# Kernel tuning notes

Hardware: AMD Instinct MI355X
Metric: run time of the kernel (lower is better)

The kernel has to match this reference:

```python
import jax, jax.numpy as jnp
import numpy as np

TOP_K = 2
BALANCE_W = 0.01


def setup_inputs() -> dict:
    key = jax.random.key(0)
    ks = jax.random.split(key, 9)
    B, T, D, E, H, S = 4, 2048, 1024, 16, 1024, 2

    def w(k, shape):
        return jax.random.normal(k, shape, jnp.float32) * 0.02

    return {
        "x": jax.random.normal(ks[0], (B, T, D), jnp.float32),
        "router_w": w(ks[1], (D, E)),
        "router_bias": jnp.zeros((E,), jnp.float32),
        "Wg": w(ks[2], (E, D, H)),
        "Wu": w(ks[3], (E, D, H)),
        "Wd": w(ks[4], (E, H, D)),
        "sWg": w(ks[5], (D, S * H)),
        "sWu": w(ks[6], (D, S * H)),
        "sWd": w(ks[7], (S * H, D)),
    }


def reference(x, router_w, router_bias, Wg, Wu, Wd, sWg, sWu, sWd):
    B, T, D = x.shape
    E = router_w.shape[1]
    flat = x.reshape(-1, D)                      # [N, D], N = B*T
    N = flat.shape[0]

    # ---- router (fp32, matching x.float() in torch ref) ----
    logits = flat @ router_w                     # [N, E]
    probs = jax.nn.softmax(logits, axis=-1)      # unbiased probs
    _, indices = jax.lax.top_k(logits + router_bias, TOP_K)  # [N, K]
    weights = jnp.take_along_axis(probs, indices, axis=-1)   # [N, K]
    weights = weights / jnp.maximum(weights.sum(-1, keepdims=True), 1e-9)

    # per-(token, expert) combine weight; top-k indices are unique per row
    C = jnp.zeros((N, E), flat.dtype).at[jnp.arange(N)[:, None], indices].add(weights)
    expert_load = jax.nn.one_hot(indices, E, dtype=jnp.float32).sum((0, 1))  # [E]

    # ---- routed SwiGLU experts: scan over experts, masked combine ----
    def body(acc, per_e):
        wg, wu, wd, c = per_e                    # [D,H],[D,H],[H,D],[N]
        h = jax.nn.silu(flat @ wg) * (flat @ wu) # [N, H]
        return acc + (h @ wd) * c[:, None], None

    routed, _ = jax.lax.scan(body, jnp.zeros_like(flat), (Wg, Wu, Wd, C.T))

    # ---- shared expert ----
    shared = (jax.nn.silu(flat @ sWg) * (flat @ sWu)) @ sWd

    out = (routed + shared).reshape(B, T, D)

    # ---- Switch/DeepSeek balance loss (training mode) ----
    expert_fraction = expert_load / (N * TOP_K)
    probability_fraction = probs.mean(0)
    balance = BALANCE_W * E * jnp.sum(expert_fraction * probability_fraction)

    return out, balance, expert_load
```

## Files before the change

### kernel.cpp

```cpp
#include <hip/hip_runtime.h>
#include <stdint.h>

#define N_TOK 8192
#define DDIM  1024
#define NEXP  16
#define HDIM  1024
#define SHDIM 2048
#define TM 128
#define BK 64
#define MT_R 144

#define SH_GU_NT  (SHDIM / 64)
#define SH_GU_WGS ((N_TOK / TM) * SH_GU_NT)
#define RT_GU_NT  (HDIM / 64)
#define RT_GU_WGS (MT_R * RT_GU_NT)
#define GU_WGS    (SH_GU_WGS + RT_GU_WGS)

#define TND 128
#define DN_NT     (DDIM / TND)
#define SH_DN_WGS ((N_TOK / TM) * DN_NT)
#define RT_DN_WGS (MT_R * DN_NT)
#define DN_WGS    (SH_DN_WGS + RT_DN_WGS)

#define CPAD 16

typedef __bf16 bf16x8 __attribute__((ext_vector_type(8)));
typedef float  f32x4  __attribute__((ext_vector_type(4)));

__device__ __forceinline__ unsigned short f2bf(float f) {
  union { float f; unsigned u; } v; v.f = f;
  unsigned r = v.u + 0x7fffu + ((v.u >> 16) & 1u);
  return (unsigned short)(r >> 16);
}

__device__ __forceinline__ void gload16(const void* g, void* l) {
  __builtin_amdgcn_global_load_lds(
      (const __attribute__((address_space(1))) void*)g,
      (__attribute__((address_space(3))) void*)l, 16, 0, 0);
}

__device__ __forceinline__ int xcd_swizzle() {
  int nwg = (int)gridDim.x;
  int b = (int)blockIdx.x;
  return (b & 7) * (nwg >> 3) + (b >> 3);
}


__global__ void k_zero(int* cnt, int* cursor, float* probsum) {
  int t = threadIdx.x;
  if (t < NEXP * CPAD) { cnt[t] = 0; cursor[t] = 0; probsum[t] = 0.f; }
}

__global__ __launch_bounds__(256) void k_router(
    const float* __restrict__ x, const float* __restrict__ rw,
    const float* __restrict__ rb, int* __restrict__ cnt,
    int* __restrict__ tok_idx, float* __restrict__ tok_w,
    float* __restrict__ probs) {
  __shared__ float rwT[NEXP * 1024];
  const int t = threadIdx.x;
  {
    int dbase = t >> 2, e0 = (t & 3) * 4;
#pragma unroll
    for (int c = 0; c < 16; c++) {
      int d = dbase + 64 * c;
      float4 v = *(const float4*)(rw + (size_t)d * NEXP + e0);
      rwT[(e0 + 0) * 1024 + d] = v.x;
      rwT[(e0 + 1) * 1024 + d] = v.y;
      rwT[(e0 + 2) * 1024 + d] = v.z;
      rwT[(e0 + 3) * 1024 + d] = v.w;
    }
  }
  __syncthreads();
  const int lane = t & 63, wv = t >> 6;
  const int tok0 = blockIdx.x * 16 + wv * 4;
  float acc[4][NEXP];
#pragma unroll
  for (int tt = 0; tt < 4; tt++)
#pragma unroll
    for (int e = 0; e < NEXP; e++) acc[tt][e] = 0.f;

#pragma unroll
  for (int c = 0; c < 4; c++) {
    int d = lane * 4 + 256 * c;
    float4 xv[4];
#pragma unroll
    for (int tt = 0; tt < 4; tt++)
      xv[tt] = *(const float4*)(x + (size_t)(tok0 + tt) * DDIM + d);
#pragma unroll
    for (int e = 0; e < NEXP; e++) {
      float4 w4 = *(const float4*)(&rwT[e * 1024 + d]);
#pragma unroll
      for (int tt = 0; tt < 4; tt++) {
        acc[tt][e] = fmaf(xv[tt].x, w4.x, acc[tt][e]);
        acc[tt][e] = fmaf(xv[tt].y, w4.y, acc[tt][e]);
        acc[tt][e] = fmaf(xv[tt].z, w4.z, acc[tt][e]);
        acc[tt][e] = fmaf(xv[tt].w, w4.w, acc[tt][e]);
      }
    }
  }
#pragma unroll
  for (int tt = 0; tt < 4; tt++)
#pragma unroll
    for (int e = 0; e < NEXP; e++) {
      float v = acc[tt][e];
#pragma unroll
      for (int o = 32; o; o >>= 1) v += __shfl_xor(v, o);
      acc[tt][e] = v;
    }

#pragma unroll
  for (int tt = 0; tt < 4; tt++) {
    if (lane == tt) {
      int tok = tok0 + tt;
      float mx = acc[tt][0];
#pragma unroll
      for (int e = 1; e < NEXP; e++) mx = fmaxf(mx, acc[tt][e]);
      float p[NEXP]; float s = 0.f;
#pragma unroll
      for (int e = 0; e < NEXP; e++) { p[e] = __expf(acc[tt][e] - mx); s += p[e]; }
      float inv = 1.f / s;
      float* pdst = probs + (size_t)tok * NEXP;
#pragma unroll
      for (int e = 0; e < NEXP; e++) { p[e] *= inv; pdst[e] = p[e]; }
      int i0 = 0; float b0 = acc[tt][0] + rb[0];
#pragma unroll
      for (int e = 1; e < NEXP; e++) { float v = acc[tt][e] + rb[e]; if (v > b0) { b0 = v; i0 = e; } }
      int i1 = -1; float b1 = -3.4e38f;
#pragma unroll
      for (int e = 0; e < NEXP; e++) {
        if (e == i0) continue;
        float v = acc[tt][e] + rb[e]; if (v > b1) { b1 = v; i1 = e; }
      }
      float w0 = 0.f, w1 = 0.f;
#pragma unroll
      for (int e = 0; e < NEXP; e++) { if (e == i0) w0 = p[e]; if (e == i1) w1 = p[e]; }
      float ssum = fmaxf(w0 + w1, 1e-9f);
      w0 /= ssum; w1 /= ssum;
      atomicAdd(&cnt[i0 * CPAD], 1); atomicAdd(&cnt[i1 * CPAD], 1);
      tok_idx[tok * 2]     = i0; tok_idx[tok * 2 + 1] = i1;
      tok_w[tok * 2]       = w0; tok_w[tok * 2 + 1]   = w1;
    }
  }
}

__global__ __launch_bounds__(256) void k_psum(
    const float* __restrict__ probs, float* __restrict__ probsum) {
  __shared__ float ps[NEXP];
  const int t = threadIdx.x;
  if (t < NEXP) ps[t] = 0.f;
  __syncthreads();
  int e = t & 15, trow = t >> 4;
  float s = 0.f;
#pragma unroll
  for (int c = 0; c < 8; c++) {
    int tok = blockIdx.x * 128 + c * 16 + trow;
    s += probs[(size_t)tok * NEXP + e];
  }
  atomicAdd(&ps[e], s);
  __syncthreads();
  if (t < NEXP) atomicAdd(&probsum[t * CPAD], ps[t]);
}

__global__ void k_prefix(const int* __restrict__ cnt, int* __restrict__ offs) {
  if (threadIdx.x == 0) {
    int o = 0;
    for (int e = 0; e < NEXP; e++) { offs[e] = o; o += ((cnt[e * CPAD] + 127) & ~127); }
    offs[NEXP] = o;
  }
}

__global__ __launch_bounds__(256) void k_assign(
    const int* __restrict__ tok_idx, const float* __restrict__ tok_w,
    int* __restrict__ cursor, const int* __restrict__ offs,
    int* __restrict__ row_token, float* __restrict__ row_w) {
  int i = blockIdx.x * 256 + threadIdx.x;
  if (i >= N_TOK * 2) return;
  int e = tok_idx[i];
  int pos = atomicAdd(&cursor[e * CPAD], 1);
  int row = offs[e] + pos;
  row_token[row] = i >> 1;
  row_w[row] = tok_w[i];
}

__global__ void k_f32_to_bf16(const float* __restrict__ src,
                              unsigned short* __restrict__ dst, int n4) {
  int i = blockIdx.x * blockDim.x + threadIdx.x;
  if (i >= n4) return;
  float4 v = ((const float4*)src)[i];
  ushort4 o;
  o.x = f2bf(v.x); o.y = f2bf(v.y); o.z = f2bf(v.z); o.w = f2bf(v.w);
  ((ushort4*)dst)[i] = o;
}

__global__ __launch_bounds__(256) void k_transpose2(
    const float* __restrict__ src, unsigned short* __restrict__ dst, int R, int C) {
  __shared__ float tile[64 * 65];
  size_t mat = (size_t)blockIdx.z * R * C;
  src += mat; dst += mat;
  int tc = blockIdx.x * 64, tr = blockIdx.y * 64;
  int rx = threadIdx.x >> 4;
  int cx = (threadIdx.x & 15) * 4;
#pragma unroll
  for (int p = 0; p < 4; p++) {
    int r = p * 16 + rx;
    float4 v = *(const float4*)(src + (size_t)(tr + r) * C + tc + cx);
    tile[(cx + 0) * 65 + r] = v.x;
    tile[(cx + 1) * 65 + r] = v.y;
    tile[(cx + 2) * 65 + r] = v.z;
    tile[(cx + 3) * 65 + r] = v.w;
  }
  __syncthreads();
#pragma unroll
  for (int p = 0; p < 4; p++) {
    int c = p * 16 + rx;
    float v0 = tile[c * 65 + cx + 0];
    float v1 = tile[c * 65 + cx + 1];
    float v2 = tile[c * 65 + cx + 2];
    float v3 = tile[c * 65 + cx + 3];
    ushort4 o; o.x = f2bf(v0); o.y = f2bf(v1); o.z = f2bf(v2); o.w = f2bf(v3);
    *(ushort4*)(dst + (size_t)(tc + c) * R + tr + cx) = o;
  }
}


__global__ __launch_bounds__(256, 4) void k_gateup_all(
    const unsigned short* __restrict__ Xbf,
    const unsigned short* __restrict__ sWgT,
    const unsigned short* __restrict__ sWuT,
    const unsigned short* __restrict__ WgT,
    const unsigned short* __restrict__ WuT,
    unsigned short* __restrict__ Hs,
    unsigned short* __restrict__ Hr,
    const int* __restrict__ offs, const int* __restrict__ cnt,
    const int* __restrict__ row_token) {
  __shared__ unsigned short As[TM * BK];
  __shared__ unsigned short Bgs[64 * BK];
  __shared__ unsigned short Bus[64 * BK];

  const int wg = xcd_swizzle();
  const int t = threadIdx.x;
  const int lane = t & 63, wv = t >> 6;
  const int lr  = lane >> 3;
  const int kbx = (lane & 7) ^ lr;

  int tm, tn, validEnd, Nh;
  const unsigned short *Bgp, *Bup;
  unsigned short* Hout;
  const unsigned short* pA[4];

  if (wg < SH_GU_WGS) {
    tm = (wg / SH_GU_NT) * TM;
    tn = (wg % SH_GU_NT) * 64;
    validEnd = 0x7fffffff;
    Bgp = sWgT; Bup = sWuT;
    Hout = Hs; Nh = SHDIM;
#pragma unroll
    for (int j = 0; j < 4; j++)
      pA[j] = Xbf + (size_t)(tm + (wv * 4 + j) * 8 + lr) * DDIM;
  } else {
    int wgr = wg - SH_GU_WGS;
    tm = (wgr / RT_GU_NT) * TM;
    tn = (wgr % RT_GU_NT) * 64;
    if (tm >= offs[NEXP]) return;
    int e = 0;
#pragma unroll
    for (int i = 1; i < NEXP; i++) if (tm >= offs[i]) e = i;
    validEnd = offs[e] + cnt[e * CPAD];
    Bgp = WgT + (size_t)e * HDIM * DDIM;
    Bup = WuT + (size_t)e * HDIM * DDIM;
    Hout = Hr; Nh = HDIM;
#pragma unroll
    for (int j = 0; j < 4; j++) {
      int row = tm + (wv * 4 + j) * 8 + lr;
      int tok = row < validEnd ? row_token[row] : 0;
      pA[j] = Xbf + (size_t)tok * DDIM;
    }
  }
  const unsigned short* pBg[2];
  const unsigned short* pBu[2];
#pragma unroll
  for (int j = 0; j < 2; j++) {
    int row = tn + (wv * 2 + j) * 8 + lr;
    pBg[j] = Bgp + (size_t)row * DDIM;
    pBu[j] = Bup + (size_t)row * DDIM;
  }

  auto stage = [&](int k0) {
#pragma unroll
    for (int j = 0; j < 4; j++)
      gload16(pA[j] + k0 + kbx * 8, (void*)&As[(wv * 4 + j) * 512]);
#pragma unroll
    for (int j = 0; j < 2; j++) {
      gload16(pBg[j] + k0 + kbx * 8, (void*)&Bgs[(wv * 2 + j) * 512]);
      gload16(pBu[j] + k0 + kbx * 8, (void*)&Bus[(wv * 2 + j) * 512]);
    }
  };

  f32x4 accG[4][2] = {};
  f32x4 accU[4][2] = {};
  const int wr = wv >> 1, wc = wv & 1;
  const int rbase = lane & 15;
  const int kgrp = lane >> 4;

  for (int k0 = 0; k0 < DDIM; k0 += BK) {
    if (k0) __syncthreads();
    stage(k0);
    __syncthreads();
#pragma unroll
    for (int kk = 0; kk < 2; kk++) {
      bf16x8 af[4], gf[2], uf[2];
      int kbl = kk * 4 + kgrp;
#pragma unroll
      for (int i = 0; i < 4; i++) {
        int r = wr * 64 + i * 16 + rbase;
        af[i] = *(const bf16x8*)((const char*)&As[0] + r * 128 + ((kbl ^ (r & 7)) << 4));
      }
#pragma unroll
      for (int j = 0; j < 2; j++) {
        int r = wc * 32 + j * 16 + rbase;
        gf[j] = *(const bf16x8*)((const char*)&Bgs[0] + r * 128 + ((kbl ^ (r & 7)) << 4));
        uf[j] = *(const bf16x8*)((const char*)&Bus[0] + r * 128 + ((kbl ^ (r & 7)) << 4));
      }
#pragma unroll
      for (int i = 0; i < 4; i++)
#pragma unroll
        for (int j = 0; j < 2; j++) {
          accG[i][j] = __builtin_amdgcn_mfma_f32_16x16x32_bf16(af[i], gf[j], accG[i][j], 0, 0, 0);
          accU[i][j] = __builtin_amdgcn_mfma_f32_16x16x32_bf16(af[i], uf[j], accU[i][j], 0, 0, 0);
        }
    }
  }

  const int orow0 = tm + wr * 64 + (lane >> 4) * 4;
  const int ocol0 = tn + wc * 32 + (lane & 15);
#pragma unroll
  for (int i = 0; i < 4; i++)
#pragma unroll
    for (int j = 0; j < 2; j++)
#pragma unroll
      for (int r = 0; r < 4; r++) {
        int row = orow0 + i * 16 + r;
        if (row < validEnd) {
          float g = accG[i][j][r], u = accU[i][j][r];
          float h = g / (1.f + __expf(-g)) * u;
          Hout[(size_t)row * Nh + ocol0 + j * 16] = f2bf(h);
        }
      }
}

__global__ __launch_bounds__(256, 4) void k_down_all(
    const unsigned short* __restrict__ Hs,
    const unsigned short* __restrict__ Hr,
    const unsigned short* __restrict__ sWdT,
    const unsigned short* __restrict__ WdT,
    float* __restrict__ out,
    const int* __restrict__ offs, const int* __restrict__ cnt,
    const int* __restrict__ row_token, const float* __restrict__ row_w) {
  __shared__ unsigned short As[TM * BK];
  __shared__ unsigned short Bs[TND * BK];

  const int wg = xcd_swizzle();
  const int t = threadIdx.x;
  const int lane = t & 63, wv = t >> 6;
  const int lr  = lane >> 3;
  const int kbx = (lane & 7) ^ lr;

  int tm, tn, validEnd, K;
  bool routed;
  const unsigned short* pA[4];
  const unsigned short* pB[4];

  if (wg < SH_DN_WGS) {
    routed = false; K = SHDIM;
    tm = (wg / DN_NT) * TM;
    tn = (wg % DN_NT) * TND;
    validEnd = 0x7fffffff;
#pragma unroll
    for (int j = 0; j < 4; j++) {
      pA[j] = Hs + (size_t)(tm + (wv * 4 + j) * 8 + lr) * SHDIM;
      pB[j] = sWdT + (size_t)(tn + (wv * 4 + j) * 8 + lr) * SHDIM;
    }
  } else {
    routed = true; K = HDIM;
    int wgr = wg - SH_DN_WGS;
    tm = (wgr / DN_NT) * TM;
    tn = (wgr % DN_NT) * TND;
    if (tm >= offs[NEXP]) return;
    int e = 0;
#pragma unroll
    for (int i = 1; i < NEXP; i++) if (tm >= offs[i]) e = i;
    validEnd = offs[e] + cnt[e * CPAD];
    const unsigned short* B = WdT + (size_t)e * DDIM * HDIM;
#pragma unroll
    for (int j = 0; j < 4; j++) {
      pA[j] = Hr + (size_t)(tm + (wv * 4 + j) * 8 + lr) * HDIM;
      pB[j] = B + (size_t)(tn + (wv * 4 + j) * 8 + lr) * HDIM;
    }
  }

  auto stage = [&](int k0) {
#pragma unroll
    for (int j = 0; j < 4; j++) {
      gload16(pA[j] + k0 + kbx * 8, (void*)&As[(wv * 4 + j) * 512]);
      gload16(pB[j] + k0 + kbx * 8, (void*)&Bs[(wv * 4 + j) * 512]);
    }
  };

  f32x4 acc[4][4] = {};
  const int wr = wv >> 1, wc = wv & 1;
  const int rbase = lane & 15;
  const int kgrp = lane >> 4;

  for (int k0 = 0; k0 < K; k0 += BK) {
    if (k0) __syncthreads();
    stage(k0);
    __syncthreads();
#pragma unroll
    for (int kk = 0; kk < 2; kk++) {
      bf16x8 af[4], bf[4];
      int kbl = kk * 4 + kgrp;
#pragma unroll
      for (int i = 0; i < 4; i++) {
        int r = wr * 64 + i * 16 + rbase;
        af[i] = *(const bf16x8*)((const char*)&As[0] + r * 128 + ((kbl ^ (r & 7)) << 4));
      }
#pragma unroll
      for (int j = 0; j < 4; j++) {
        int r = wc * 64 + j * 16 + rbase;
        bf[j] = *(const bf16x8*)((const char*)&Bs[0] + r * 128 + ((kbl ^ (r & 7)) << 4));
      }
#pragma unroll
      for (int i = 0; i < 4; i++)
#pragma unroll
        for (int j = 0; j < 4; j++)
          acc[i][j] = __builtin_amdgcn_mfma_f32_16x16x32_bf16(af[i], bf[j], acc[i][j], 0, 0, 0);
    }
  }

  const int orow0 = tm + wr * 64 + (lane >> 4) * 4;
  const int ocol0 = tn + wc * 64 + (lane & 15);
#pragma unroll
  for (int i = 0; i < 4; i++)
#pragma unroll
    for (int j = 0; j < 4; j++)
#pragma unroll
      for (int r = 0; r < 4; r++) {
        int row = orow0 + i * 16 + r;
        int col = ocol0 + j * 16;
        if (row < validEnd) {
          int tok; float wgt;
          if (routed) { tok = row_token[row]; wgt = row_w[row]; }
          else        { tok = row;            wgt = 1.f; }
          atomicAdd(&out[(size_t)tok * DDIM + col], acc[i][j][r] * wgt);
        }
      }
}

__global__ void k_tail(const float* __restrict__ probsum, const int* __restrict__ cnt,
                       float* __restrict__ out_tail) {
  if (threadIdx.x == 0) {
    float bal = 0.f;
    for (int e = 0; e < NEXP; e++) {
      float frac = (float)cnt[e * CPAD] / (float)(N_TOK * 2);
      bal += frac * (probsum[e * CPAD] / (float)N_TOK);
    }
    out_tail[0] = 0.01f * (float)NEXP * bal;
  }
  if (threadIdx.x < NEXP) out_tail[1 + threadIdx.x] = (float)cnt[threadIdx.x * CPAD];
}


extern "C" void kernel_launch(void* const* d_in, const int* in_sizes, int n_in,
                              void* d_out, int out_size, void* d_ws, size_t ws_size,
                              hipStream_t stream) {
  const float* x   = (const float*)d_in[0];
  const float* rw  = (const float*)d_in[1];
  const float* rb  = (const float*)d_in[2];
  const float* Wg  = (const float*)d_in[3];
  const float* Wu  = (const float*)d_in[4];
  const float* Wd  = (const float*)d_in[5];
  const float* sWg = (const float*)d_in[6];
  const float* sWu = (const float*)d_in[7];
  const float* sWd = (const float*)d_in[8];
  float* out = (float*)d_out;

  uint8_t* w = (uint8_t*)d_ws;
  size_t off = 0;
  auto alloc = [&](size_t bytes) -> void* {
    void* p = w + off;
    off += (bytes + 255) & ~(size_t)255;
    return p;
  };

  int*   cnt     = (int*)alloc(NEXP * CPAD * 4);
  int*   cursor  = (int*)alloc(NEXP * CPAD * 4);
  float* probsum = (float*)alloc(NEXP * CPAD * 4);
  int*   offs    = (int*)alloc((NEXP + 1) * 4);
  int*   tok_idx = (int*)alloc((size_t)N_TOK * 2 * 4);
  float* tok_w   = (float*)alloc((size_t)N_TOK * 2 * 4);
  int*   row_tok = (int*)alloc((size_t)MT_R * TM * 4);
  float* row_w   = (float*)alloc((size_t)MT_R * TM * 4);
  float* probs   = (float*)alloc((size_t)N_TOK * NEXP * 4);
  unsigned short* Xbf  = (unsigned short*)alloc((size_t)N_TOK * DDIM * 2);
  unsigned short* Hs   = (unsigned short*)alloc((size_t)N_TOK * SHDIM * 2);
  unsigned short* Hr   = (unsigned short*)alloc((size_t)MT_R * TM * HDIM * 2);
  unsigned short* WgT  = (unsigned short*)alloc((size_t)NEXP * HDIM * DDIM * 2);
  unsigned short* WuT  = (unsigned short*)alloc((size_t)NEXP * HDIM * DDIM * 2);
  unsigned short* WdT  = (unsigned short*)alloc((size_t)NEXP * DDIM * HDIM * 2);
  unsigned short* sWgT = (unsigned short*)alloc((size_t)SHDIM * DDIM * 2);
  unsigned short* sWuT = (unsigned short*)alloc((size_t)SHDIM * DDIM * 2);
  unsigned short* sWdT = (unsigned short*)alloc((size_t)DDIM * SHDIM * 2);

  if (off > ws_size) return;

  k_zero<<<1, 256, 0, stream>>>(cnt, cursor, probsum);
  k_router<<<N_TOK / 16, 256, 0, stream>>>(x, rw, rb, cnt, tok_idx, tok_w, probs);
  k_psum<<<64, 256, 0, stream>>>(probs, probsum);
  k_prefix<<<1, 1, 0, stream>>>(cnt, offs);
  k_assign<<<(N_TOK * 2) / 256, 256, 0, stream>>>(tok_idx, tok_w, cursor, offs, row_tok, row_w);
  k_f32_to_bf16<<<(N_TOK * DDIM / 4 + 255) / 256, 256, 0, stream>>>(x, Xbf, N_TOK * DDIM / 4);

  k_transpose2<<<dim3(HDIM / 64, DDIM / 64, NEXP), 256, 0, stream>>>(Wg, WgT, DDIM, HDIM);
  k_transpose2<<<dim3(HDIM / 64, DDIM / 64, NEXP), 256, 0, stream>>>(Wu, WuT, DDIM, HDIM);
  k_transpose2<<<dim3(DDIM / 64, HDIM / 64, NEXP), 256, 0, stream>>>(Wd, WdT, HDIM, DDIM);
  k_transpose2<<<dim3(SHDIM / 64, DDIM / 64, 1), 256, 0, stream>>>(sWg, sWgT, DDIM, SHDIM);
  k_transpose2<<<dim3(SHDIM / 64, DDIM / 64, 1), 256, 0, stream>>>(sWu, sWuT, DDIM, SHDIM);
  k_transpose2<<<dim3(DDIM / 64, SHDIM / 64, 1), 256, 0, stream>>>(sWd, sWdT, SHDIM, DDIM);

  hipMemsetAsync(out, 0, (size_t)N_TOK * DDIM * 4, stream);

  k_gateup_all<<<GU_WGS, 256, 0, stream>>>(
      Xbf, sWgT, sWuT, WgT, WuT, Hs, Hr, offs, cnt, row_tok);
  k_down_all<<<DN_WGS, 256, 0, stream>>>(
      Hs, Hr, sWdT, WdT, out, offs, cnt, row_tok, row_w);

  k_tail<<<1, 32, 0, stream>>>(probsum, cnt, out + (size_t)N_TOK * DDIM);
}
```

Measured before the change: 472.7 us.

## Replace atomic scatter with bf16 routed buffer and combine kernel; fuse prep kernels

Several changes land together. The x-to-bf16 conversion is folded into the router, and the six weight transposes collapse into two launches. The down projection now writes shared output directly and routed rows to a bf16 buffer, which a new per-token combine kernel reads back. This removes the memset and the fp32 atomics. The gate/up tile ordering is also banded so neighbouring workgroups share B tiles. In exchange there is an extra global round trip and the routed partials are rounded to bf16.

```diff
diff --git a/kernel.cpp b/kernel.cpp
--- a/kernel.cpp
+++ b/kernel.cpp
@@ -32,6 +32,9 @@
   unsigned r = v.u + 0x7fffu + ((v.u >> 16) & 1u);
   return (unsigned short)(r >> 16);
 }
+__device__ __forceinline__ float bf2f(unsigned short u) {
+  union { unsigned u; float f; } v; v.u = (unsigned)u << 16; return v.f;
+}
 
 __device__ __forceinline__ void gload16(const void* g, void* l) {
   __builtin_amdgcn_global_load_lds(
@@ -55,7 +58,7 @@
     const float* __restrict__ x, const float* __restrict__ rw,
     const float* __restrict__ rb, int* __restrict__ cnt,
     int* __restrict__ tok_idx, float* __restrict__ tok_w,
-    float* __restrict__ probs) {
+    float* __restrict__ probs, unsigned short* __restrict__ Xbf) {
   __shared__ float rwT[NEXP * 1024];
   const int t = threadIdx.x;
   {
@@ -84,8 +87,13 @@
     int d = lane * 4 + 256 * c;
     float4 xv[4];
 #pragma unroll
-    for (int tt = 0; tt < 4; tt++)
+    for (int tt = 0; tt < 4; tt++) {
       xv[tt] = *(const float4*)(x + (size_t)(tok0 + tt) * DDIM + d);
+      ushort4 o;
+      o.x = f2bf(xv[tt].x); o.y = f2bf(xv[tt].y);
+      o.z = f2bf(xv[tt].z); o.w = f2bf(xv[tt].w);
+      *(ushort4*)(Xbf + (size_t)(tok0 + tt) * DDIM + d) = o;
+    }
 #pragma unroll
     for (int e = 0; e < NEXP; e++) {
       float4 w4 = *(const float4*)(&rwT[e * 1024 + d]);
@@ -172,32 +180,20 @@
 __global__ __launch_bounds__(256) void k_assign(
     const int* __restrict__ tok_idx, const float* __restrict__ tok_w,
     int* __restrict__ cursor, const int* __restrict__ offs,
-    int* __restrict__ row_token, float* __restrict__ row_w) {
+    int* __restrict__ row_token, int* __restrict__ tok_rows) {
   int i = blockIdx.x * 256 + threadIdx.x;
   if (i >= N_TOK * 2) return;
   int e = tok_idx[i];
   int pos = atomicAdd(&cursor[e * CPAD], 1);
   int row = offs[e] + pos;
   row_token[row] = i >> 1;
-  row_w[row] = tok_w[i];
-}
-
-__global__ void k_f32_to_bf16(const float* __restrict__ src,
-                              unsigned short* __restrict__ dst, int n4) {
-  int i = blockIdx.x * blockDim.x + threadIdx.x;
-  if (i >= n4) return;
-  float4 v = ((const float4*)src)[i];
-  ushort4 o;
-  o.x = f2bf(v.x); o.y = f2bf(v.y); o.z = f2bf(v.z); o.w = f2bf(v.w);
-  ((ushort4*)dst)[i] = o;
-}
-
-__global__ __launch_bounds__(256) void k_transpose2(
-    const float* __restrict__ src, unsigned short* __restrict__ dst, int R, int C) {
-  __shared__ float tile[64 * 65];
-  size_t mat = (size_t)blockIdx.z * R * C;
-  src += mat; dst += mat;
-  int tc = blockIdx.x * 64, tr = blockIdx.y * 64;
+  tok_rows[i] = row;
+}
+
+
+__device__ __forceinline__ void do_transpose64(
+    const float* __restrict__ src, unsigned short* __restrict__ dst,
+    int R, int C, int tc, int tr, float* tile ) {
   int rx = threadIdx.x >> 4;
   int cx = (threadIdx.x & 15) * 4;
 #pragma unroll
@@ -219,6 +215,41 @@
     float v3 = tile[c * 65 + cx + 3];
     ushort4 o; o.x = f2bf(v0); o.y = f2bf(v1); o.z = f2bf(v2); o.w = f2bf(v3);
     *(ushort4*)(dst + (size_t)(tc + c) * R + tr + cx) = o;
+  }
+}
+
+__global__ __launch_bounds__(256) void k_transpose_big(
+    const float* __restrict__ Wg, const float* __restrict__ Wu,
+    const float* __restrict__ Wd, unsigned short* __restrict__ WgT,
+    unsigned short* __restrict__ WuT, unsigned short* __restrict__ WdT) {
+  __shared__ float tile[64 * 65];
+  int id = blockIdx.x;
+  int which = id >> 12;
+  int rem = id & 4095;
+  int mat = rem >> 8;
+  int tl  = rem & 255;
+  int bx = tl & 15, by = tl >> 4;
+  const float* src = (which == 0 ? Wg : which == 1 ? Wu : Wd) + (size_t)mat * 1024 * 1024;
+  unsigned short* dst = (which == 0 ? WgT : which == 1 ? WuT : WdT) + (size_t)mat * 1024 * 1024;
+  do_transpose64(src, dst, 1024, 1024, bx * 64, by * 64, tile);
+}
+
+__global__ __launch_bounds__(256) void k_transpose_sh(
+    const float* __restrict__ sWg, const float* __restrict__ sWu,
+    const float* __restrict__ sWd, unsigned short* __restrict__ sWgT,
+    unsigned short* __restrict__ sWuT, unsigned short* __restrict__ sWdT) {
+  __shared__ float tile[64 * 65];
+  int id = blockIdx.x;
+  if (id < 1024) {
+    const float* src = id < 512 ? sWg : sWu;
+    unsigned short* dst = id < 512 ? sWgT : sWuT;
+    int tl = id & 511;
+    int bx = tl & 31, by = tl >> 5;
+    do_transpose64(src, dst, 1024, 2048, bx * 64, by * 64, tile);
+  } else {
+    int tl = id - 1024;
+    int bx = tl & 15, by = tl >> 4;
+    do_transpose64(sWd, sWdT, 2048, 1024, bx * 64, by * 64, tile);
   }
 }
 
@@ -249,8 +280,10 @@
   const unsigned short* pA[4];
 
   if (wg < SH_GU_WGS) {
-    tm = (wg / SH_GU_NT) * TM;
-    tn = (wg % SH_GU_NT) * 64;
+    int band = wg >> 9;
+    int r = wg & 511;
+    tm = (r >> 3) * TM;
+    tn = (band * 8 + (r & 7)) * 64;
     validEnd = 0x7fffffff;
     Bgp = sWgT; Bup = sWuT;
     Hout = Hs; Nh = SHDIM;
@@ -258,9 +291,11 @@
     for (int j = 0; j < 4; j++)
       pA[j] = Xbf + (size_t)(tm + (wv * 4 + j) * 8 + lr) * DDIM;
   } else {
-    int wgr = wg - SH_GU_WGS;
-    tm = (wgr / RT_GU_NT) * TM;
-    tn = (wgr % RT_GU_NT) * 64;
+    int u = wg - SH_GU_WGS;
+    int band = u / 1152;
+    int r = u % 1152;
+    tm = (r >> 3) * TM;
+    tn = (band * 8 + (r & 7)) * 64;
     if (tm >= offs[NEXP]) return;
     int e = 0;
 #pragma unroll
@@ -354,8 +389,8 @@
     const unsigned short* __restrict__ sWdT,
     const unsigned short* __restrict__ WdT,
     float* __restrict__ out,
-    const int* __restrict__ offs, const int* __restrict__ cnt,
-    const int* __restrict__ row_token, const float* __restrict__ row_w) {
+    unsigned short* __restrict__ Rbuf,
+    const int* __restrict__ offs, const int* __restrict__ cnt) {
   __shared__ unsigned short As[TM * BK];
   __shared__ unsigned short Bs[TND * BK];
 
@@ -372,8 +407,8 @@
 
   if (wg < SH_DN_WGS) {
     routed = false; K = SHDIM;
-    tm = (wg / DN_NT) * TM;
-    tn = (wg % DN_NT) * TND;
+    tm = (wg >> 3) * TM;
+    tn = (wg & 7) * TND;
     validEnd = 0x7fffffff;
 #pragma unroll
     for (int j = 0; j < 4; j++) {
@@ -383,8 +418,8 @@
   } else {
     routed = true; K = HDIM;
     int wgr = wg - SH_DN_WGS;
-    tm = (wgr / DN_NT) * TM;
-    tn = (wgr % DN_NT) * TND;
+    tm = (wgr >> 3) * TM;
+    tn = (wgr & 7) * TND;
     if (tm >= offs[NEXP]) return;
     int e = 0;
 #pragma unroll
@@ -447,13 +482,29 @@
       for (int r = 0; r < 4; r++) {
         int row = orow0 + i * 16 + r;
         int col = ocol0 + j * 16;
-        if (row < validEnd) {
-          int tok; float wgt;
-          if (routed) { tok = row_token[row]; wgt = row_w[row]; }
-          else        { tok = row;            wgt = 1.f; }
-          atomicAdd(&out[(size_t)tok * DDIM + col], acc[i][j][r] * wgt);
+        if (routed) {
+          if (row < validEnd) Rbuf[(size_t)row * DDIM + col] = f2bf(acc[i][j][r]);
+        } else {
+          out[(size_t)row * DDIM + col] = acc[i][j][r];
         }
       }
+}
+
+__global__ __launch_bounds__(256) void k_combine(
+    float* __restrict__ out, const unsigned short* __restrict__ Rbuf,
+    const int* __restrict__ tok_rows, const float* __restrict__ tok_w) {
+  int tok = blockIdx.x;
+  int c = threadIdx.x;
+  int r0 = tok_rows[tok * 2], r1 = tok_rows[tok * 2 + 1];
+  float w0 = tok_w[tok * 2],  w1 = tok_w[tok * 2 + 1];
+  float4 o  = ((const float4*)(out + (size_t)tok * DDIM))[c];
+  ushort4 a = ((const ushort4*)(Rbuf + (size_t)r0 * DDIM))[c];
+  ushort4 b = ((const ushort4*)(Rbuf + (size_t)r1 * DDIM))[c];
+  o.x += w0 * bf2f(a.x) + w1 * bf2f(b.x);
+  o.y += w0 * bf2f(a.y) + w1 * bf2f(b.y);
+  o.z += w0 * bf2f(a.z) + w1 * bf2f(b.z);
+  o.w += w0 * bf2f(a.w) + w1 * bf2f(b.w);
+  ((float4*)(out + (size_t)tok * DDIM))[c] = o;
 }
 
 __global__ void k_tail(const float* __restrict__ probsum, const int* __restrict__ cnt,
@@ -492,18 +543,19 @@
     return p;
   };
 
-  int*   cnt     = (int*)alloc(NEXP * CPAD * 4);
-  int*   cursor  = (int*)alloc(NEXP * CPAD * 4);
-  float* probsum = (float*)alloc(NEXP * CPAD * 4);
-  int*   offs    = (int*)alloc((NEXP + 1) * 4);
-  int*   tok_idx = (int*)alloc((size_t)N_TOK * 2 * 4);
-  float* tok_w   = (float*)alloc((size_t)N_TOK * 2 * 4);
-  int*   row_tok = (int*)alloc((size_t)MT_R * TM * 4);
-  float* row_w   = (float*)alloc((size_t)MT_R * TM * 4);
-  float* probs   = (float*)alloc((size_t)N_TOK * NEXP * 4);
+  int*   cnt      = (int*)alloc(NEXP * CPAD * 4);
+  int*   cursor   = (int*)alloc(NEXP * CPAD * 4);
+  float* probsum  = (float*)alloc(NEXP * CPAD * 4);
+  int*   offs     = (int*)alloc((NEXP + 1) * 4);
+  int*   tok_idx  = (int*)alloc((size_t)N_TOK * 2 * 4);
+  float* tok_w    = (float*)alloc((size_t)N_TOK * 2 * 4);
+  int*   tok_rows = (int*)alloc((size_t)N_TOK * 2 * 4);
+  int*   row_tok  = (int*)alloc((size_t)MT_R * TM * 4);
+  float* probs    = (float*)alloc((size_t)N_TOK * NEXP * 4);
   unsigned short* Xbf  = (unsigned short*)alloc((size_t)N_TOK * DDIM * 2);
   unsigned short* Hs   = (unsigned short*)alloc((size_t)N_TOK * SHDIM * 2);
   unsigned short* Hr   = (unsigned short*)alloc((size_t)MT_R * TM * HDIM * 2);
+  unsigned short* Rbuf = (unsigned short*)alloc((size_t)MT_R * TM * DDIM * 2);
   unsigned short* WgT  = (unsigned short*)alloc((size_t)NEXP * HDIM * DDIM * 2);
   unsigned short* WuT  = (unsigned short*)alloc((size_t)NEXP * HDIM * DDIM * 2);
   unsigned short* WdT  = (unsigned short*)alloc((size_t)NEXP * DDIM * HDIM * 2);
@@ -514,25 +566,19 @@
   if (off > ws_size) return;
 
   k_zero<<<1, 256, 0, stream>>>(cnt, cursor, probsum);
-  k_router<<<N_TOK / 16, 256, 0, stream>>>(x, rw, rb, cnt, tok_idx, tok_w, probs);
+  k_router<<<N_TOK / 16, 256, 0, stream>>>(x, rw, rb, cnt, tok_idx, tok_w, probs, Xbf);
   k_psum<<<64, 256, 0, stream>>>(probs, probsum);
   k_prefix<<<1, 1, 0, stream>>>(cnt, offs);
-  k_assign<<<(N_TOK * 2) / 256, 256, 0, stream>>>(tok_idx, tok_w, cursor, offs, row_tok, row_w);
-  k_f32_to_bf16<<<(N_TOK * DDIM / 4 + 255) / 256, 256, 0, stream>>>(x, Xbf, N_TOK * DDIM / 4);
-
-  k_transpose2<<<dim3(HDIM / 64, DDIM / 64, NEXP), 256, 0, stream>>>(Wg, WgT, DDIM, HDIM);
-  k_transpose2<<<dim3(HDIM / 64, DDIM / 64, NEXP), 256, 0, stream>>>(Wu, WuT, DDIM, HDIM);
-  k_transpose2<<<dim3(DDIM / 64, HDIM / 64, NEXP), 256, 0, stream>>>(Wd, WdT, HDIM, DDIM);
-  k_transpose2<<<dim3(SHDIM / 64, DDIM / 64, 1), 256, 0, stream>>>(sWg, sWgT, DDIM, SHDIM);
-  k_transpose2<<<dim3(SHDIM / 64, DDIM / 64, 1), 256, 0, stream>>>(sWu, sWuT, DDIM, SHDIM);
-  k_transpose2<<<dim3(DDIM / 64, SHDIM / 64, 1), 256, 0, stream>>>(sWd, sWdT, SHDIM, DDIM);
-
-  hipMemsetAsync(out, 0, (size_t)N_TOK * DDIM * 4, stream);
+  k_assign<<<(N_TOK * 2) / 256, 256, 0, stream>>>(tok_idx, tok_w, cursor, offs, row_tok, tok_rows);
+
+  k_transpose_big<<<12288, 256, 0, stream>>>(Wg, Wu, Wd, WgT, WuT, WdT);
+  k_transpose_sh<<<1536, 256, 0, stream>>>(sWg, sWu, sWd, sWgT, sWuT, sWdT);
 
   k_gateup_all<<<GU_WGS, 256, 0, stream>>>(
       Xbf, sWgT, sWuT, WgT, WuT, Hs, Hr, offs, cnt, row_tok);
   k_down_all<<<DN_WGS, 256, 0, stream>>>(
-      Hs, Hr, sWdT, WdT, out, offs, cnt, row_tok, row_w);
+      Hs, Hr, sWdT, WdT, out, Rbuf, offs, cnt);
+  k_combine<<<N_TOK, 256, 0, stream>>>(out, Rbuf, tok_rows, tok_w);
 
   k_tail<<<1, 32, 0, stream>>>(probsum, cnt, out + (size_t)N_TOK * DDIM);
 }
```

After: 426.5 us. -9.8%, faster.
